# Optimization experiments

Measured on AMD Instinct MI355X. Metric: run time of the kernel, lower is better.

## Reference

```python
import jax, jax.numpy as jnp
import numpy as np

N_NODES = 50000
N_EDGES = 800000
IN_CH = 128
OUT_CH = 64
HID = 2 * OUT_CH  # 128
NEG_SLOPE = 0.2  # PyG GATConv default negative_slope


def gat_conv(x, edge_index, W, a_src, a_dst, b):
    """Single-head PyG GATConv (heads=1, concat=True, self-loops already in edge_index)."""
    N = x.shape[0]
    h = x @ W  # [N, C]
    src, dst = edge_index[0], edge_index[1]
    # per-edge attention logits: leaky_relu(a_src . h_src + a_dst . h_dst)
    e = jax.nn.leaky_relu((h @ a_src)[src] + (h @ a_dst)[dst], NEG_SLOPE)  # [E]
    # softmax over incoming edges of each dst node (numerically stable)
    m = jax.ops.segment_max(e, dst, num_segments=N)
    p = jnp.exp(e - m[dst])
    denom = jax.ops.segment_sum(p, dst, num_segments=N)
    coef = p / denom[dst]  # [E]
    # scatter-aggregate weighted source features
    out = jax.ops.segment_sum(coef[:, None] * h[src], dst, num_segments=N)  # [N, C]
    return out + b


def setup_inputs() -> dict:
    key = jax.random.key(0)
    ks = jax.random.split(key, 12)
    s_in = 1.0 / np.sqrt(IN_CH)
    s_h = 1.0 / np.sqrt(HID)
    return {
        "x": jax.random.normal(ks[0], (N_NODES, IN_CH), dtype=jnp.float32),
        "edge_index": jax.random.randint(ks[1], (2, N_EDGES), 0, N_NODES, dtype=jnp.int64),
        "W1": jax.random.normal(ks[2], (IN_CH, HID), dtype=jnp.float32) * s_in,
        "a_src1": jax.random.normal(ks[3], (HID,), dtype=jnp.float32) * s_h,
        "a_dst1": jax.random.normal(ks[4], (HID,), dtype=jnp.float32) * s_h,
        "b1": jnp.zeros((HID,), dtype=jnp.float32),
        "W_mu": jax.random.normal(ks[5], (HID, OUT_CH), dtype=jnp.float32) * s_h,
        "a_src_mu": jax.random.normal(ks[6], (OUT_CH,), dtype=jnp.float32) * 0.125,
        "a_dst_mu": jax.random.normal(ks[7], (OUT_CH,), dtype=jnp.float32) * 0.125,
        "b_mu": jnp.zeros((OUT_CH,), dtype=jnp.float32),
        "W_ls": jax.random.normal(ks[8], (HID, OUT_CH), dtype=jnp.float32) * s_h,
        "a_src_ls": jax.random.normal(ks[9], (OUT_CH,), dtype=jnp.float32) * 0.125,
        "a_dst_ls": jax.random.normal(ks[10], (OUT_CH,), dtype=jnp.float32) * 0.125,
        "b_ls": jnp.zeros((OUT_CH,), dtype=jnp.float32),
    }


def reference(x, edge_index, W1, a_src1, a_dst1, b1, W_mu, a_src_mu, a_dst_mu, b_mu, W_ls, a_src_ls, a_dst_ls, b_ls):
    N = x.shape[0]
    loops = jnp.arange(N, dtype=edge_index.dtype)
    ei = jnp.concatenate([edge_index, jnp.stack([loops, loops])], axis=1)  # add self-loops
    h = jax.nn.relu(gat_conv(x, ei, W1, a_src1, a_dst1, b1))
    mu = gat_conv(h, ei, W_mu, a_src_mu, a_dst_mu, b_mu)
    logstd = gat_conv(h, ei, W_ls, a_src_ls, a_dst_ls, b_ls)
    return mu, logstd
```

## Files before the change

### kernel.cpp

```cpp
#include <hip/hip_runtime.h>
#include <hip/hip_bf16.h>
#include <math.h>

typedef __attribute__((ext_vector_type(8))) _Float16 half8;
typedef __attribute__((ext_vector_type(4))) float f32x4;


__device__ __forceinline__ float leaky02(float v) { return v > 0.0f ? v : 0.2f * v; }

__device__ __forceinline__ unsigned short f2bf(float f) {
  unsigned u = __float_as_uint(f);
  u += 0x7FFF + ((u >> 16) & 1);
  return (unsigned short)(u >> 16);
}
__device__ __forceinline__ float2 bfp(unsigned v) {
  float2 r;
  r.x = __uint_as_float(v << 16);
  r.y = __uint_as_float(v & 0xFFFF0000u);
  return r;
}


#define BSHIFT 8
#define BDSTS 256

#define CHUNK 4096
__global__ __launch_bounds__(256) void pair_scatter_kernel(
    const int* __restrict__ ei, int* __restrict__ bcursor, unsigned* __restrict__ pairs, int E) {
  __shared__ int h[256], base[256], cur[256];
  h[threadIdx.x] = 0; cur[threadIdx.x] = 0;
  __syncthreads();
  int c0 = blockIdx.x * CHUNK;
  int c1 = min(c0 + CHUNK, E);
  for (int e = c0 + (int)threadIdx.x; e < c1; e += 256)
    atomicAdd(&h[ei[E + e] >> BSHIFT], 1);
  __syncthreads();
  if (h[threadIdx.x])
    base[threadIdx.x] = atomicAdd(&bcursor[threadIdx.x], h[threadIdx.x]);
  __syncthreads();
  for (int e = c0 + (int)threadIdx.x; e < c1; e += 256) {
    int dst = ei[E + e];
    int src = ei[e];
    int b = dst >> BSHIFT;
    int r = atomicAdd(&cur[b], 1);
    pairs[base[b] + r] = ((unsigned)src << BSHIFT) | (unsigned)(dst & (BDSTS - 1));
  }
}

__global__ __launch_bounds__(256) void fine_kernel(
    const unsigned* __restrict__ pairs, const int* __restrict__ bstart,
    int* __restrict__ row_start, int* __restrict__ esrc, int N) {
  __shared__ int h[BDSTS], sc[BDSTS], cur[BDSTS];
  int t = threadIdx.x;
  int b = blockIdx.x;
  int d0 = b << BSHIFT;
  int beg = bstart[b], end = bstart[b + 1];
  h[t] = 0;
  __syncthreads();
  for (int i = beg + t; i < end; i += 256) atomicAdd(&h[pairs[i] & (BDSTS - 1)], 1);
  __syncthreads();
  int v = h[t];
  sc[t] = v;
  __syncthreads();
#pragma unroll
  for (int off = 1; off < BDSTS; off <<= 1) {
    int tmp = (t >= off) ? sc[t - off] : 0;
    __syncthreads();
    sc[t] += tmp;
    __syncthreads();
  }
  int excl = sc[t] - v;
  if (d0 + t < N) row_start[d0 + t] = beg + excl;
  cur[t] = excl;
  __syncthreads();
  for (int i = beg + t; i < end; i += 256) {
    unsigned p = pairs[i];
    int r = atomicAdd(&cur[p & (BDSTS - 1)], 1);
    esrc[beg + r] = (int)(p >> BSHIFT);
  }
}


__global__ __launch_bounds__(256) void prep_w_kernel(
    const float* __restrict__ W1, const float* __restrict__ Wmu, const float* __restrict__ Wls,
    _Float16* __restrict__ Wt1, _Float16* __restrict__ Wt2,
    int* __restrict__ bcount, int* __restrict__ done, int NBUCK) {
  int idx = blockIdx.x * 256 + threadIdx.x;
  int c = idx >> 7, k = idx & 127;
  Wt1[idx] = (_Float16)W1[k * 128 + c];
  float w2 = (c < 64) ? Wmu[k * 64 + c] : Wls[k * 64 + (c - 64)];
  Wt2[idx] = (_Float16)w2;
  if (blockIdx.x == 0) {
    if ((int)threadIdx.x <= NBUCK) bcount[threadIdx.x] = 0;
    if (threadIdx.x == 255) *done = 0;
  }
}


__global__ __launch_bounds__(256) void gemm1_hist(
    const float* __restrict__ X, const _Float16* __restrict__ Wt,
    const float* __restrict__ a_src, const float* __restrict__ a_dst,
    unsigned short* __restrict__ Hb, float* __restrict__ asrc, float* __restrict__ adst, int N,
    const int* __restrict__ ei, int* __restrict__ bcount, int E, int nGB, int nHB,
    int* __restrict__ bstart, int* __restrict__ bcursor, int* __restrict__ row_start,
    int* __restrict__ done, int NBUCK) {
  if ((int)blockIdx.x >= nGB) {
    __shared__ int h[256];
    __shared__ int lastFlag;
    h[threadIdx.x] = 0;
    __syncthreads();
    int hb = (int)blockIdx.x - nGB;
    int c0 = hb * 2048;
    int c1 = min(c0 + 2048, E);
    for (int e = c0 + (int)threadIdx.x; e < c1; e += 256)
      atomicAdd(&h[ei[E + e] >> BSHIFT], 1);
    __syncthreads();
    if (h[threadIdx.x]) atomicAdd(&bcount[threadIdx.x], h[threadIdx.x]);
    __syncthreads();
    if (threadIdx.x == 0) {
      __threadfence();
      lastFlag = (atomicAdd(done, 1) == nHB - 1) ? 1 : 0;
    }
    __syncthreads();
    if (lastFlag) {
      int t = threadIdx.x;
      int v = (t < NBUCK) ? atomicAdd(&bcount[t], 0) : 0;
      h[t] = v;
      __syncthreads();
#pragma unroll
      for (int off = 1; off < 256; off <<= 1) {
        int tmp = (t >= off) ? h[t - off] : 0;
        __syncthreads();
        h[t] += tmp;
        __syncthreads();
      }
      if (t < NBUCK) {
        int excl = h[t] - v;
        bstart[t] = excl;
        bcursor[t] = excl;
      }
      if (t == 0) { bstart[NBUCK] = E; row_start[N] = E; }
    }
    return;
  }
  const int wid = threadIdx.x >> 6, lane = threadIdx.x & 63;
  const int r16 = ((int)blockIdx.x * 4 + wid) * 16;
  if (r16 >= N) return;
  const int cg = lane & 15;
  const int kq = (lane >> 4) * 8;
  const int rowClamp = min(r16 + cg, N - 1);

  f32x4 acc[8];
#pragma unroll
  for (int j = 0; j < 8; ++j) acc[j] = (f32x4){0.f, 0.f, 0.f, 0.f};

#pragma unroll
  for (int ks = 0; ks < 4; ++ks) {
    const int k0 = ks * 32;
    const float* xp = X + (size_t)rowClamp * 128 + k0 + kq;
    float4 xa = *(const float4*)xp;
    float4 xb = *(const float4*)(xp + 4);
    half8 a;
    a[0] = (_Float16)xa.x; a[1] = (_Float16)xa.y; a[2] = (_Float16)xa.z; a[3] = (_Float16)xa.w;
    a[4] = (_Float16)xb.x; a[5] = (_Float16)xb.y; a[6] = (_Float16)xb.z; a[7] = (_Float16)xb.w;
#pragma unroll
    for (int j = 0; j < 8; ++j) {
      half8 b = *(const half8*)(Wt + (size_t)(16 * j + cg) * 128 + k0 + kq);
      acc[j] = __builtin_amdgcn_mfma_f32_16x16x32_f16(a, b, acc[j], 0, 0, 0);
    }
  }

  float as_[8], ds_[8];
#pragma unroll
  for (int j = 0; j < 8; ++j) { as_[j] = a_src[16 * j + cg]; ds_[j] = a_dst[16 * j + cg]; }
  const int rg = (lane >> 4) * 4;
#pragma unroll
  for (int reg = 0; reg < 4; ++reg) {
    int row = r16 + rg + reg;
    bool ok = row < N;
    float ps = 0.f, pd = 0.f;
#pragma unroll
    for (int j = 0; j < 8; ++j) {
      float v = acc[j][reg];
      if (ok) Hb[(size_t)row * 128 + 16 * j + cg] = f2bf(v);
      ps = fmaf(v, as_[j], ps);
      pd = fmaf(v, ds_[j], pd);
    }
#pragma unroll
    for (int o = 1; o < 16; o <<= 1) { ps += __shfl_xor(ps, o); pd += __shfl_xor(pd, o); }
    if (ok && cg == 0) { asrc[row] = ps; adst[row] = pd; }
  }
}

__global__ __launch_bounds__(256) void gemm2_mfma(
    const _Float16* __restrict__ Xh, const _Float16* __restrict__ Wt,
    const float* __restrict__ a_src_mu, const float* __restrict__ a_dst_mu,
    const float* __restrict__ a_src_ls, const float* __restrict__ a_dst_ls,
    unsigned short* __restrict__ Hb, float* __restrict__ as2, float* __restrict__ ad2, int N) {
  const int wid = threadIdx.x >> 6, lane = threadIdx.x & 63;
  const int r16 = ((int)blockIdx.x * 4 + wid) * 16;
  if (r16 >= N) return;
  const int cg = lane & 15;
  const int kq = (lane >> 4) * 8;
  const int rowClamp = min(r16 + cg, N - 1);

  f32x4 acc[8];
#pragma unroll
  for (int j = 0; j < 8; ++j) acc[j] = (f32x4){0.f, 0.f, 0.f, 0.f};

#pragma unroll
  for (int ks = 0; ks < 4; ++ks) {
    const int k0 = ks * 32;
    half8 a = *(const half8*)(Xh + (size_t)rowClamp * 128 + k0 + kq);
#pragma unroll
    for (int j = 0; j < 8; ++j) {
      half8 b = *(const half8*)(Wt + (size_t)(16 * j + cg) * 128 + k0 + kq);
      acc[j] = __builtin_amdgcn_mfma_f32_16x16x32_f16(a, b, acc[j], 0, 0, 0);
    }
  }

  float asv[8], adv[8];
#pragma unroll
  for (int j = 0; j < 4; ++j) {
    asv[j] = a_src_mu[16 * j + cg]; adv[j] = a_dst_mu[16 * j + cg];
    asv[j + 4] = a_src_ls[16 * j + cg]; adv[j + 4] = a_dst_ls[16 * j + cg];
  }
  const int rg = (lane >> 4) * 4;
#pragma unroll
  for (int reg = 0; reg < 4; ++reg) {
    int row = r16 + rg + reg;
    bool ok = row < N;
    float psm = 0.f, pdm = 0.f, psl = 0.f, pdl = 0.f;
#pragma unroll
    for (int j = 0; j < 8; ++j) {
      float v = acc[j][reg];
      if (ok) Hb[(size_t)row * 128 + 16 * j + cg] = f2bf(v);
      if (j < 4) { psm = fmaf(v, asv[j], psm); pdm = fmaf(v, adv[j], pdm); }
      else       { psl = fmaf(v, asv[j], psl); pdl = fmaf(v, adv[j], pdl); }
    }
#pragma unroll
    for (int o = 1; o < 16; o <<= 1) {
      psm += __shfl_xor(psm, o); pdm += __shfl_xor(pdm, o);
      psl += __shfl_xor(psl, o); pdl += __shfl_xor(pdl, o);
    }
    if (ok && cg == 0) {
      as2[2 * row] = psm; ad2[2 * row] = pdm;
      as2[2 * row + 1] = psl; ad2[2 * row + 1] = pdl;
    }
  }
}


#define STEP1(J)                                                          \
  {                                                                       \
    int idx = (J) + grp;                                                  \
    int sA = __shfl(s, hbase + idx);                                      \
    float wA = __shfl(w, hbase + idx);                                    \
    uint4 hv = *(const uint4*)(Hb + (size_t)sA * 128 + li * 8);           \
    float2 q0 = bfp(hv.x), q1 = bfp(hv.y), q2 = bfp(hv.z), q3 = bfp(hv.w);\
    a0 = fmaf(wA, q0.x, a0); a1 = fmaf(wA, q0.y, a1);                     \
    a2 = fmaf(wA, q1.x, a2); a3 = fmaf(wA, q1.y, a3);                     \
    a4 = fmaf(wA, q2.x, a4); a5 = fmaf(wA, q2.y, a5);                     \
    a6 = fmaf(wA, q3.x, a6); a7 = fmaf(wA, q3.y, a7);                     \
  }

__global__ __launch_bounds__(256) void agg1_g16(
    const unsigned short* __restrict__ Hb, const float* __restrict__ asrc,
    const float* __restrict__ adst, const int* __restrict__ row_start,
    const int* __restrict__ esrc, const float* __restrict__ b,
    _Float16* __restrict__ hout, int N) {
  const int lane = threadIdx.x & 63;
  const int half = lane >> 5, sub = lane & 31;
  const int grp = (lane >> 4) & 1, li = lane & 15;
  const int g = (int)(blockIdx.x * 4 + (threadIdx.x >> 6));
  const int d = g * 2 + half;
  const bool dok = d < N;
  const int dc = dok ? d : N - 1;
  const float ad = adst[dc];
  const float wself = __expf(leaky02(asrc[dc] + ad));
  float a0 = 0.f, a1 = 0.f, a2 = 0.f, a3 = 0.f, a4 = 0.f, a5 = 0.f, a6 = 0.f, a7 = 0.f;
  if (grp == 0) {
    uint4 sv = *(const uint4*)(Hb + (size_t)dc * 128 + li * 8);
    float2 q0 = bfp(sv.x), q1 = bfp(sv.y), q2 = bfp(sv.z), q3 = bfp(sv.w);
    a0 = wself * q0.x; a1 = wself * q0.y; a2 = wself * q1.x; a3 = wself * q1.y;
    a4 = wself * q2.x; a5 = wself * q2.y; a6 = wself * q3.x; a7 = wself * q3.y;
  }
  float den = (sub == 0) ? wself : 0.f;
  const int beg = row_start[dc];
  const int n = dok ? (row_start[dc + 1] - beg) : 0;
  const int nmax = max(n, __shfl_xor(n, 32));
  const int hbase = half * 32;
  for (int c0 = 0; c0 < nmax; c0 += 32) {
    int j = c0 + sub;
    bool v = j < n;
    int s = v ? esrc[beg + j] : 0;
    float w = v ? __expf(leaky02(asrc[s] + ad)) : 0.f;
    den += w;
    int cnt = n - c0;
    cnt = min(max(cnt, 0), 32);
    int jj = 0;
    for (; jj + 8 <= cnt; jj += 8) { STEP1(jj) STEP1(jj + 2) STEP1(jj + 4) STEP1(jj + 6) }
    for (; jj < cnt; jj += 2) {
      int idx = jj + grp;
      int sA = __shfl(s, hbase + idx);
      float wA = __shfl(w, hbase + idx);
      if (idx < cnt) {
        uint4 hv = *(const uint4*)(Hb + (size_t)sA * 128 + li * 8);
        float2 q0 = bfp(hv.x), q1 = bfp(hv.y), q2 = bfp(hv.z), q3 = bfp(hv.w);
        a0 = fmaf(wA, q0.x, a0); a1 = fmaf(wA, q0.y, a1);
        a2 = fmaf(wA, q1.x, a2); a3 = fmaf(wA, q1.y, a3);
        a4 = fmaf(wA, q2.x, a4); a5 = fmaf(wA, q2.y, a5);
        a6 = fmaf(wA, q3.x, a6); a7 = fmaf(wA, q3.y, a7);
      }
    }
  }
  a0 += __shfl_xor(a0, 16); a1 += __shfl_xor(a1, 16);
  a2 += __shfl_xor(a2, 16); a3 += __shfl_xor(a3, 16);
  a4 += __shfl_xor(a4, 16); a5 += __shfl_xor(a5, 16);
  a6 += __shfl_xor(a6, 16); a7 += __shfl_xor(a7, 16);
#pragma unroll
  for (int o = 16; o > 0; o >>= 1) den += __shfl_xor(den, o);
  if (dok && grp == 0) {
    float inv = 1.0f / den;
    float4 b0 = *(const float4*)(b + li * 8);
    float4 b1 = *(const float4*)(b + li * 8 + 4);
    _Float16 o8[8];
    o8[0] = (_Float16)fmaxf(fmaf(a0, inv, b0.x), 0.f);
    o8[1] = (_Float16)fmaxf(fmaf(a1, inv, b0.y), 0.f);
    o8[2] = (_Float16)fmaxf(fmaf(a2, inv, b0.z), 0.f);
    o8[3] = (_Float16)fmaxf(fmaf(a3, inv, b0.w), 0.f);
    o8[4] = (_Float16)fmaxf(fmaf(a4, inv, b1.x), 0.f);
    o8[5] = (_Float16)fmaxf(fmaf(a5, inv, b1.y), 0.f);
    o8[6] = (_Float16)fmaxf(fmaf(a6, inv, b1.z), 0.f);
    o8[7] = (_Float16)fmaxf(fmaf(a7, inv, b1.w), 0.f);
    *(uint4*)(hout + (size_t)d * 128 + li * 8) = *(uint4*)o8;
  }
}


#define STEP2(J)                                                          \
  {                                                                       \
    int idx = (J) + grp;                                                  \
    int sA = __shfl(s, hbase + idx);                                      \
    float wmA = __shfl(wm, hbase + idx);                                  \
    float wlA = __shfl(wl, hbase + idx);                                  \
    float wA = isMu ? wmA : wlA;                                          \
    uint4 hv = *(const uint4*)(Hb + (size_t)sA * 128 + li * 8);           \
    float2 q0 = bfp(hv.x), q1 = bfp(hv.y), q2 = bfp(hv.z), q3 = bfp(hv.w);\
    a0 = fmaf(wA, q0.x, a0); a1 = fmaf(wA, q0.y, a1);                     \
    a2 = fmaf(wA, q1.x, a2); a3 = fmaf(wA, q1.y, a3);                     \
    a4 = fmaf(wA, q2.x, a4); a5 = fmaf(wA, q2.y, a5);                     \
    a6 = fmaf(wA, q3.x, a6); a7 = fmaf(wA, q3.y, a7);                     \
  }

__global__ __launch_bounds__(256) void agg2_g16(
    const unsigned short* __restrict__ Hb,
    const float2* __restrict__ as2, const float2* __restrict__ ad2,
    const int* __restrict__ row_start, const int* __restrict__ esrc,
    const float* __restrict__ b_mu, const float* __restrict__ b_ls,
    float* __restrict__ out_mu, float* __restrict__ out_ls, int N) {
  const int lane = threadIdx.x & 63;
  const int half = lane >> 5, sub = lane & 31;
  const int grp = (lane >> 4) & 1, li = lane & 15;
  const bool isMu = li < 8;
  const int g = (int)(blockIdx.x * 4 + (threadIdx.x >> 6));
  const int d = g * 2 + half;
  const bool dok = d < N;
  const int dc = dok ? d : N - 1;
  const float2 adv = ad2[dc];
  const float2 asv = as2[dc];
  const float wself_m = __expf(leaky02(asv.x + adv.x));
  const float wself_l = __expf(leaky02(asv.y + adv.y));
  float a0 = 0.f, a1 = 0.f, a2 = 0.f, a3 = 0.f, a4 = 0.f, a5 = 0.f, a6 = 0.f, a7 = 0.f;
  if (grp == 0) {
    const float wself = isMu ? wself_m : wself_l;
    uint4 sv = *(const uint4*)(Hb + (size_t)dc * 128 + li * 8);
    float2 q0 = bfp(sv.x), q1 = bfp(sv.y), q2 = bfp(sv.z), q3 = bfp(sv.w);
    a0 = wself * q0.x; a1 = wself * q0.y; a2 = wself * q1.x; a3 = wself * q1.y;
    a4 = wself * q2.x; a5 = wself * q2.y; a6 = wself * q3.x; a7 = wself * q3.y;
  }
  float den_m = (sub == 0) ? wself_m : 0.f;
  float den_l = (sub == 0) ? wself_l : 0.f;
  const int beg = row_start[dc];
  const int n = dok ? (row_start[dc + 1] - beg) : 0;
  const int nmax = max(n, __shfl_xor(n, 32));
  const int hbase = half * 32;
  for (int c0 = 0; c0 < nmax; c0 += 32) {
    int j = c0 + sub;
    bool v = j < n;
    int s = v ? esrc[beg + j] : 0;
    float wm = 0.f, wl = 0.f;
    if (v) {
      float2 av = as2[s];
      wm = __expf(leaky02(av.x + adv.x));
      wl = __expf(leaky02(av.y + adv.y));
    }
    den_m += wm;
    den_l += wl;
    int cnt = n - c0;
    cnt = min(max(cnt, 0), 32);
    int jj = 0;
    for (; jj + 8 <= cnt; jj += 8) { STEP2(jj) STEP2(jj + 2) STEP2(jj + 4) STEP2(jj + 6) }
    for (; jj < cnt; jj += 2) {
      int idx = jj + grp;
      int sA = __shfl(s, hbase + idx);
      float wmA = __shfl(wm, hbase + idx);
      float wlA = __shfl(wl, hbase + idx);
      float wA = isMu ? wmA : wlA;
      if (idx < cnt) {
        uint4 hv = *(const uint4*)(Hb + (size_t)sA * 128 + li * 8);
        float2 q0 = bfp(hv.x), q1 = bfp(hv.y), q2 = bfp(hv.z), q3 = bfp(hv.w);
        a0 = fmaf(wA, q0.x, a0); a1 = fmaf(wA, q0.y, a1);
        a2 = fmaf(wA, q1.x, a2); a3 = fmaf(wA, q1.y, a3);
        a4 = fmaf(wA, q2.x, a4); a5 = fmaf(wA, q2.y, a5);
        a6 = fmaf(wA, q3.x, a6); a7 = fmaf(wA, q3.y, a7);
      }
    }
  }
  a0 += __shfl_xor(a0, 16); a1 += __shfl_xor(a1, 16);
  a2 += __shfl_xor(a2, 16); a3 += __shfl_xor(a3, 16);
  a4 += __shfl_xor(a4, 16); a5 += __shfl_xor(a5, 16);
  a6 += __shfl_xor(a6, 16); a7 += __shfl_xor(a7, 16);
#pragma unroll
  for (int o = 16; o > 0; o >>= 1) {
    den_m += __shfl_xor(den_m, o);
    den_l += __shfl_xor(den_l, o);
  }
  if (dok && grp == 0) {
    float inv = isMu ? (1.0f / den_m) : (1.0f / den_l);
    const float* bp;
    float* op;
    if (isMu) { bp = b_mu + li * 8; op = out_mu + (size_t)d * 64 + li * 8; }
    else      { bp = b_ls + (li - 8) * 8; op = out_ls + (size_t)d * 64 + (li - 8) * 8; }
    float4 b0 = *(const float4*)bp;
    float4 b1 = *(const float4*)(bp + 4);
    float4 o0, o1;
    o0.x = fmaf(a0, inv, b0.x); o0.y = fmaf(a1, inv, b0.y);
    o0.z = fmaf(a2, inv, b0.z); o0.w = fmaf(a3, inv, b0.w);
    o1.x = fmaf(a4, inv, b1.x); o1.y = fmaf(a5, inv, b1.y);
    o1.z = fmaf(a6, inv, b1.z); o1.w = fmaf(a7, inv, b1.w);
    *(float4*)op = o0;
    *(float4*)(op + 4) = o1;
  }
}


extern "C" void kernel_launch(void* const* d_in, const int* in_sizes, int n_in,
                              void* d_out, int out_size, void* d_ws, size_t ws_size,
                              hipStream_t stream) {
  const float* x = (const float*)d_in[0];
  const int* ei = (const int*)d_in[1];
  const float* W1 = (const float*)d_in[2];
  const float* a_src1 = (const float*)d_in[3];
  const float* a_dst1 = (const float*)d_in[4];
  const float* b1 = (const float*)d_in[5];
  const float* W_mu = (const float*)d_in[6];
  const float* a_src_mu = (const float*)d_in[7];
  const float* a_dst_mu = (const float*)d_in[8];
  const float* b_mu = (const float*)d_in[9];
  const float* W_ls = (const float*)d_in[10];
  const float* a_src_ls = (const float*)d_in[11];
  const float* a_dst_ls = (const float*)d_in[12];
  const float* b_ls = (const float*)d_in[13];

  const int N = in_sizes[0] / 128;
  const int E = in_sizes[1] / 2;
  const int NBUCK = (N + BDSTS - 1) >> BSHIFT;

  uint8_t* p = (uint8_t*)d_ws;
  auto carve = [&](size_t bytes) -> void* {
    void* q = (void*)p;
    p += (bytes + 255) & ~(size_t)255;
    return q;
  };
  int* bcount = (int*)carve((size_t)(NBUCK + 1) * 4);
  int* bstart = (int*)carve((size_t)(NBUCK + 1) * 4);
  int* bcursor = (int*)carve((size_t)NBUCK * 4);
  int* done = (int*)carve(4);
  int* row_start = (int*)carve((size_t)(N + 1) * 4);
  int* esrc = (int*)carve((size_t)E * 4);
  unsigned* pairs = (unsigned*)carve((size_t)E * 4);
  unsigned short* Hb1 = (unsigned short*)carve((size_t)N * 128 * 2);
  _Float16* h1 = (_Float16*)carve((size_t)N * 128 * 2);
  _Float16* Wt1 = (_Float16*)carve((size_t)128 * 128 * 2);
  _Float16* Wt2 = (_Float16*)carve((size_t)128 * 128 * 2);
  float* as1 = (float*)carve((size_t)N * 4);
  float* ad1 = (float*)carve((size_t)N * 4);
  float* as2 = (float*)carve((size_t)N * 8);
  float* ad2 = (float*)carve((size_t)N * 8);

  unsigned short* Hb2 = Hb1;

  prep_w_kernel<<<64, 256, 0, stream>>>(W1, W_mu, W_ls, Wt1, Wt2, bcount, done, NBUCK);

  const int nGB = (N + 63) / 64;
  const int nHB = (E + 2047) / 2048;
  gemm1_hist<<<nGB + nHB, 256, 0, stream>>>(x, Wt1, a_src1, a_dst1, Hb1, as1, ad1, N,
                                            ei, bcount, E, nGB, nHB,
                                            bstart, bcursor, row_start, done, NBUCK);
  pair_scatter_kernel<<<(E + CHUNK - 1) / CHUNK, 256, 0, stream>>>(ei, bcursor, pairs, E);
  fine_kernel<<<NBUCK, 256, 0, stream>>>(pairs, bstart, row_start, esrc, N);

  const int nwaves = (N + 1) / 2;
  const int nblk = (nwaves + 3) / 4;
  agg1_g16<<<nblk, 256, 0, stream>>>(Hb1, as1, ad1, row_start, esrc, b1, h1, N);
  gemm2_mfma<<<(N + 63) / 64, 256, 0, stream>>>(h1, Wt2, a_src_mu, a_dst_mu,
                                                a_src_ls, a_dst_ls, Hb2, as2, ad2, N);
  float* out_mu = (float*)d_out;
  float* out_ls = out_mu + (size_t)N * 64;
  agg2_g16<<<nblk, 256, 0, stream>>>(Hb2, (const float2*)as2, (const float2*)ad2,
                                     row_start, esrc, b_mu, b_ls, out_mu, out_ls, N);
}
```

Baseline: 161.3 us.

## Regroup preprocessing: fuse weight prep with histogram, gemm1 with pair scatter

Moves the destination-bucket histogram and scan out of the gemm1 launch and into the weight-transpose launch. The pair-scatter pass is then merged into the gemm1 launch as extra blocks. The goal is to overlap the scatter work with the first GEMM and keep the same number of launches as before the scatter kernel was separate. A memset now zeroes the counters in place of the prep kernel, which adds one memset node on the stream.

```diff
diff --git a/kernel.cpp b/kernel.cpp
--- a/kernel.cpp
+++ b/kernel.cpp
@@ -20,32 +20,141 @@
   return r;
 }
 
-
 #define BSHIFT 8
 #define BDSTS 256
-
 #define CHUNK 4096
-__global__ __launch_bounds__(256) void pair_scatter_kernel(
-    const int* __restrict__ ei, int* __restrict__ bcursor, unsigned* __restrict__ pairs, int E) {
-  __shared__ int h[256], base[256], cur[256];
-  h[threadIdx.x] = 0; cur[threadIdx.x] = 0;
-  __syncthreads();
-  int c0 = blockIdx.x * CHUNK;
-  int c1 = min(c0 + CHUNK, E);
+
+
+__global__ __launch_bounds__(256) void prep_hist(
+    const float* __restrict__ W1, const float* __restrict__ Wmu, const float* __restrict__ Wls,
+    _Float16* __restrict__ Wt1, _Float16* __restrict__ Wt2,
+    const int* __restrict__ ei, int* __restrict__ bcount, int E, int nPB, int nHB,
+    int* __restrict__ bstart, int* __restrict__ bcursor, int* __restrict__ row_start,
+    int* __restrict__ done, int NBUCK, int N) {
+  if ((int)blockIdx.x < nPB) {
+    int idx = blockIdx.x * 256 + threadIdx.x;
+    int c = idx >> 7, k = idx & 127;
+    Wt1[idx] = (_Float16)W1[k * 128 + c];
+    float w2 = (c < 64) ? Wmu[k * 64 + c] : Wls[k * 64 + (c - 64)];
+    Wt2[idx] = (_Float16)w2;
+    return;
+  }
+  __shared__ int h[256];
+  __shared__ int lastFlag;
+  h[threadIdx.x] = 0;
+  __syncthreads();
+  int hb = (int)blockIdx.x - nPB;
+  int c0 = hb * 2048;
+  int c1 = min(c0 + 2048, E);
   for (int e = c0 + (int)threadIdx.x; e < c1; e += 256)
     atomicAdd(&h[ei[E + e] >> BSHIFT], 1);
   __syncthreads();
-  if (h[threadIdx.x])
-    base[threadIdx.x] = atomicAdd(&bcursor[threadIdx.x], h[threadIdx.x]);
-  __syncthreads();
-  for (int e = c0 + (int)threadIdx.x; e < c1; e += 256) {
-    int dst = ei[E + e];
-    int src = ei[e];
-    int b = dst >> BSHIFT;
-    int r = atomicAdd(&cur[b], 1);
-    pairs[base[b] + r] = ((unsigned)src << BSHIFT) | (unsigned)(dst & (BDSTS - 1));
-  }
-}
+  if (h[threadIdx.x]) atomicAdd(&bcount[threadIdx.x], h[threadIdx.x]);
+  __syncthreads();
+  if (threadIdx.x == 0) {
+    __threadfence();
+    lastFlag = (atomicAdd(done, 1) == nHB - 1) ? 1 : 0;
+  }
+  __syncthreads();
+  if (lastFlag) {
+    int t = threadIdx.x;
+    int v = (t < NBUCK) ? atomicAdd(&bcount[t], 0) : 0;
+    h[t] = v;
+    __syncthreads();
+#pragma unroll
+    for (int off = 1; off < 256; off <<= 1) {
+      int tmp = (t >= off) ? h[t - off] : 0;
+      __syncthreads();
+      h[t] += tmp;
+      __syncthreads();
+    }
+    if (t < NBUCK) {
+      int excl = h[t] - v;
+      bstart[t] = excl;
+      bcursor[t] = excl;
+    }
+    if (t == 0) { bstart[NBUCK] = E; row_start[N] = E; }
+  }
+}
+
+
+__global__ __launch_bounds__(256) void gemm1_scatter(
+    const float* __restrict__ X, const _Float16* __restrict__ Wt,
+    const float* __restrict__ a_src, const float* __restrict__ a_dst,
+    unsigned short* __restrict__ Hb, float* __restrict__ asrc, float* __restrict__ adst, int N,
+    const int* __restrict__ ei, int* __restrict__ bcursor, unsigned* __restrict__ pairs,
+    int E, int nGB) {
+  if ((int)blockIdx.x >= nGB) {
+    __shared__ int h[256], base[256], cur[256];
+    h[threadIdx.x] = 0; cur[threadIdx.x] = 0;
+    __syncthreads();
+    int sb = (int)blockIdx.x - nGB;
+    int c0 = sb * CHUNK;
+    int c1 = min(c0 + CHUNK, E);
+    for (int e = c0 + (int)threadIdx.x; e < c1; e += 256)
+      atomicAdd(&h[ei[E + e] >> BSHIFT], 1);
+    __syncthreads();
+    if (h[threadIdx.x])
+      base[threadIdx.x] = atomicAdd(&bcursor[threadIdx.x], h[threadIdx.x]);
+    __syncthreads();
+    for (int e = c0 + (int)threadIdx.x; e < c1; e += 256) {
+      int dst = ei[E + e];
+      int src = ei[e];
+      int b = dst >> BSHIFT;
+      int r = atomicAdd(&cur[b], 1);
+      pairs[base[b] + r] = ((unsigned)src << BSHIFT) | (unsigned)(dst & (BDSTS - 1));
+    }
+    return;
+  }
+  const int wid = threadIdx.x >> 6, lane = threadIdx.x & 63;
+  const int r16 = ((int)blockIdx.x * 4 + wid) * 16;
+  if (r16 >= N) return;
+  const int cg = lane & 15;
+  const int kq = (lane >> 4) * 8;
+  const int rowClamp = min(r16 + cg, N - 1);
+
+  f32x4 acc[8];
+#pragma unroll
+  for (int j = 0; j < 8; ++j) acc[j] = (f32x4){0.f, 0.f, 0.f, 0.f};
+
+#pragma unroll
+  for (int ks = 0; ks < 4; ++ks) {
+    const int k0 = ks * 32;
+    const float* xp = X + (size_t)rowClamp * 128 + k0 + kq;
+    float4 xa = *(const float4*)xp;
+    float4 xb = *(const float4*)(xp + 4);
+    half8 a;
+    a[0] = (_Float16)xa.x; a[1] = (_Float16)xa.y; a[2] = (_Float16)xa.z; a[3] = (_Float16)xa.w;
+    a[4] = (_Float16)xb.x; a[5] = (_Float16)xb.y; a[6] = (_Float16)xb.z; a[7] = (_Float16)xb.w;
+#pragma unroll
+    for (int j = 0; j < 8; ++j) {
+      half8 b = *(const half8*)(Wt + (size_t)(16 * j + cg) * 128 + k0 + kq);
+      acc[j] = __builtin_amdgcn_mfma_f32_16x16x32_f16(a, b, acc[j], 0, 0, 0);
+    }
+  }
+
+  float as_[8], ds_[8];
+#pragma unroll
+  for (int j = 0; j < 8; ++j) { as_[j] = a_src[16 * j + cg]; ds_[j] = a_dst[16 * j + cg]; }
+  const int rg = (lane >> 4) * 4;
+#pragma unroll
+  for (int reg = 0; reg < 4; ++reg) {
+    int row = r16 + rg + reg;
+    bool ok = row < N;
+    float ps = 0.f, pd = 0.f;
+#pragma unroll
+    for (int j = 0; j < 8; ++j) {
+      float v = acc[j][reg];
+      if (ok) Hb[(size_t)row * 128 + 16 * j + cg] = f2bf(v);
+      ps = fmaf(v, as_[j], ps);
+      pd = fmaf(v, ds_[j], pd);
+    }
+#pragma unroll
+    for (int o = 1; o < 16; o <<= 1) { ps += __shfl_xor(ps, o); pd += __shfl_xor(pd, o); }
+    if (ok && cg == 0) { asrc[row] = ps; adst[row] = pd; }
+  }
+}
+
 
 __global__ __launch_bounds__(256) void fine_kernel(
     const unsigned* __restrict__ pairs, const int* __restrict__ bstart,
@@ -80,117 +189,6 @@
   }
 }
 
-
-__global__ __launch_bounds__(256) void prep_w_kernel(
-    const float* __restrict__ W1, const float* __restrict__ Wmu, const float* __restrict__ Wls,
-    _Float16* __restrict__ Wt1, _Float16* __restrict__ Wt2,
-    int* __restrict__ bcount, int* __restrict__ done, int NBUCK) {
-  int idx = blockIdx.x * 256 + threadIdx.x;
-  int c = idx >> 7, k = idx & 127;
-  Wt1[idx] = (_Float16)W1[k * 128 + c];
-  float w2 = (c < 64) ? Wmu[k * 64 + c] : Wls[k * 64 + (c - 64)];
-  Wt2[idx] = (_Float16)w2;
-  if (blockIdx.x == 0) {
-    if ((int)threadIdx.x <= NBUCK) bcount[threadIdx.x] = 0;
-    if (threadIdx.x == 255) *done = 0;
-  }
-}
-
-
-__global__ __launch_bounds__(256) void gemm1_hist(
-    const float* __restrict__ X, const _Float16* __restrict__ Wt,
-    const float* __restrict__ a_src, const float* __restrict__ a_dst,
-    unsigned short* __restrict__ Hb, float* __restrict__ asrc, float* __restrict__ adst, int N,
-    const int* __restrict__ ei, int* __restrict__ bcount, int E, int nGB, int nHB,
-    int* __restrict__ bstart, int* __restrict__ bcursor, int* __restrict__ row_start,
-    int* __restrict__ done, int NBUCK) {
-  if ((int)blockIdx.x >= nGB) {
-    __shared__ int h[256];
-    __shared__ int lastFlag;
-    h[threadIdx.x] = 0;
-    __syncthreads();
-    int hb = (int)blockIdx.x - nGB;
-    int c0 = hb * 2048;
-    int c1 = min(c0 + 2048, E);
-    for (int e = c0 + (int)threadIdx.x; e < c1; e += 256)
-      atomicAdd(&h[ei[E + e] >> BSHIFT], 1);
-    __syncthreads();
-    if (h[threadIdx.x]) atomicAdd(&bcount[threadIdx.x], h[threadIdx.x]);
-    __syncthreads();
-    if (threadIdx.x == 0) {
-      __threadfence();
-      lastFlag = (atomicAdd(done, 1) == nHB - 1) ? 1 : 0;
-    }
-    __syncthreads();
-    if (lastFlag) {
-      int t = threadIdx.x;
-      int v = (t < NBUCK) ? atomicAdd(&bcount[t], 0) : 0;
-      h[t] = v;
-      __syncthreads();
-#pragma unroll
-      for (int off = 1; off < 256; off <<= 1) {
-        int tmp = (t >= off) ? h[t - off] : 0;
-        __syncthreads();
-        h[t] += tmp;
-        __syncthreads();
-      }
-      if (t < NBUCK) {
-        int excl = h[t] - v;
-        bstart[t] = excl;
-        bcursor[t] = excl;
-      }
-      if (t == 0) { bstart[NBUCK] = E; row_start[N] = E; }
-    }
-    return;
-  }
-  const int wid = threadIdx.x >> 6, lane = threadIdx.x & 63;
-  const int r16 = ((int)blockIdx.x * 4 + wid) * 16;
-  if (r16 >= N) return;
-  const int cg = lane & 15;
-  const int kq = (lane >> 4) * 8;
-  const int rowClamp = min(r16 + cg, N - 1);
-
-  f32x4 acc[8];
-#pragma unroll
-  for (int j = 0; j < 8; ++j) acc[j] = (f32x4){0.f, 0.f, 0.f, 0.f};
-
-#pragma unroll
-  for (int ks = 0; ks < 4; ++ks) {
-    const int k0 = ks * 32;
-    const float* xp = X + (size_t)rowClamp * 128 + k0 + kq;
-    float4 xa = *(const float4*)xp;
-    float4 xb = *(const float4*)(xp + 4);
-    half8 a;
-    a[0] = (_Float16)xa.x; a[1] = (_Float16)xa.y; a[2] = (_Float16)xa.z; a[3] = (_Float16)xa.w;
-    a[4] = (_Float16)xb.x; a[5] = (_Float16)xb.y; a[6] = (_Float16)xb.z; a[7] = (_Float16)xb.w;
-#pragma unroll
-    for (int j = 0; j < 8; ++j) {
-      half8 b = *(const half8*)(Wt + (size_t)(16 * j + cg) * 128 + k0 + kq);
-      acc[j] = __builtin_amdgcn_mfma_f32_16x16x32_f16(a, b, acc[j], 0, 0, 0);
-    }
-  }
-
-  float as_[8], ds_[8];
-#pragma unroll
-  for (int j = 0; j < 8; ++j) { as_[j] = a_src[16 * j + cg]; ds_[j] = a_dst[16 * j + cg]; }
-  const int rg = (lane >> 4) * 4;
-#pragma unroll
-  for (int reg = 0; reg < 4; ++reg) {
-    int row = r16 + rg + reg;
-    bool ok = row < N;
-    float ps = 0.f, pd = 0.f;
-#pragma unroll
-    for (int j = 0; j < 8; ++j) {
-      float v = acc[j][reg];
-      if (ok) Hb[(size_t)row * 128 + 16 * j + cg] = f2bf(v);
-      ps = fmaf(v, as_[j], ps);
-      pd = fmaf(v, ds_[j], pd);
-    }
-#pragma unroll
-    for (int o = 1; o < 16; o <<= 1) { ps += __shfl_xor(ps, o); pd += __shfl_xor(pd, o); }
-    if (ok && cg == 0) { asrc[row] = ps; adst[row] = pd; }
-  }
-}
 
 __global__ __launch_bounds__(256) void gemm2_mfma(
     const _Float16* __restrict__ Xh, const _Float16* __restrict__ Wt,
@@ -296,8 +294,7 @@
     int s = v ? esrc[beg + j] : 0;
     float w = v ? __expf(leaky02(asrc[s] + ad)) : 0.f;
     den += w;
-    int cnt = n - c0;
-    cnt = min(max(cnt, 0), 32);
+    int cnt = min(max(n - c0, 0), 32);
     int jj = 0;
     for (; jj + 8 <= cnt; jj += 8) { STEP1(jj) STEP1(jj + 2) STEP1(jj + 4) STEP1(jj + 6) }
     for (; jj < cnt; jj += 2) {
@@ -397,8 +394,7 @@
     }
     den_m += wm;
     den_l += wl;
-    int cnt = n - c0;
-    cnt = min(max(cnt, 0), 32);
+    int cnt = min(max(n - c0, 0), 32);
     int jj = 0;
     for (; jj + 8 <= cnt; jj += 8) { STEP2(jj) STEP2(jj + 2) STEP2(jj + 4) STEP2(jj + 6) }
     for (; jj < cnt; jj += 2) {
@@ -473,10 +469,10 @@
     p += (bytes + 255) & ~(size_t)255;
     return q;
   };
-  int* bcount = (int*)carve((size_t)(NBUCK + 1) * 4);
+  int* bcount = (int*)carve((size_t)(NBUCK + 2) * 4);
+  int* done = bcount + NBUCK + 1;
   int* bstart = (int*)carve((size_t)(NBUCK + 1) * 4);
   int* bcursor = (int*)carve((size_t)NBUCK * 4);
-  int* done = (int*)carve(4);
   int* row_start = (int*)carve((size_t)(N + 1) * 4);
   int* esrc = (int*)carve((size_t)E * 4);
   unsigned* pairs = (unsigned*)carve((size_t)E * 4);
@@ -491,14 +487,18 @@
 
   unsigned short* Hb2 = Hb1;
 
-  prep_w_kernel<<<64, 256, 0, stream>>>(W1, W_mu, W_ls, Wt1, Wt2, bcount, done, NBUCK);
+  hipMemsetAsync(bcount, 0, (size_t)(NBUCK + 2) * 4, stream);
+
+  const int nPB = 64;
+  const int nHB = (E + 2047) / 2048;
+  prep_hist<<<nPB + nHB, 256, 0, stream>>>(W1, W_mu, W_ls, Wt1, Wt2,
+                                           ei, bcount, E, nPB, nHB,
+                                           bstart, bcursor, row_start, done, NBUCK, N);
 
   const int nGB = (N + 63) / 64;
-  const int nHB = (E + 2047) / 2048;
-  gemm1_hist<<<nGB + nHB, 256, 0, stream>>>(x, Wt1, a_src1, a_dst1, Hb1, as1, ad1, N,
-                                            ei, bcount, E, nGB, nHB,
-                                            bstart, bcursor, row_start, done, NBUCK);
-  pair_scatter_kernel<<<(E + CHUNK - 1) / CHUNK, 256, 0, stream>>>(ei, bcursor, pairs, E);
+  const int nSC = (E + CHUNK - 1) / CHUNK;
+  gemm1_scatter<<<nGB + nSC, 256, 0, stream>>>(x, Wt1, a_src1, a_dst1, Hb1, as1, ad1, N,
+                                               ei, bcursor, pairs, E, nGB);
   fine_kernel<<<NBUCK, 256, 0, stream>>>(pairs, bstart, row_start, esrc, N);
 
   const int nwaves = (N + 1) / 2;
```

After: 155.9 us, median of 2. 1.03x faster.
